# Optimization experiments

Measured on AMD Instinct MI355X. Metric: run time of the kernel, lower is better.

Reference implementation:

```python
import jax, jax.numpy as jnp
import numpy as np

B, NQ, NK, D, H, DH = 4, 2048, 2048, 512, 8, 64  # inner_dim = H*DH = 512 = query_dim


def setup_inputs() -> dict:
    key = jax.random.key(0)
    ks = jax.random.split(key, 9)
    s = 0.02
    return {
        "init_query": jax.random.normal(ks[0], (B, NQ, D), dtype=jnp.float32),
        "embedding": jax.random.normal(ks[1], (B, NK, D), dtype=jnp.float32),
        "Wq": jax.random.normal(ks[2], (D, H * DH), dtype=jnp.float32) * s,
        "Wk": jax.random.normal(ks[3], (D, H * DH), dtype=jnp.float32) * s,
        "Wv": jax.random.normal(ks[4], (D, H * DH), dtype=jnp.float32) * s,
        "W0": jax.random.normal(ks[5], (H * DH, D), dtype=jnp.float32) * s,
        "b0": jnp.zeros((D,), dtype=jnp.float32),
        "W1": jax.random.normal(ks[6], (D, D), dtype=jnp.float32) * s,
        "b1": jnp.zeros((D,), dtype=jnp.float32),
    }


def reference(init_query, embedding, Wq, Wk, Wv, W0, b0, W1, b1):
    b, nq, _ = init_query.shape
    nk = embedding.shape[1]
    # project and split heads -> [b, h, n, dh]
    q = (init_query @ Wq).reshape(b, nq, H, DH).transpose(0, 2, 1, 3)
    k = (embedding @ Wk).reshape(b, nk, H, DH).transpose(0, 2, 1, 3)
    v = (embedding @ Wv).reshape(b, nk, H, DH).transpose(0, 2, 1, 3)
    # offset attention: alpha=1 (no 1/sqrt(d) scale)
    scores = jnp.einsum("bhqd,bhkd->bhqk", q, k)
    # softmax over the QUERY axis (torch dim=1 of [B*H, Nq, Nk]), then renormalize rows
    probs = jax.nn.softmax(scores, axis=2)
    probs = probs / (1e-12 + probs.sum(axis=-1, keepdims=True))
    out = jnp.einsum("bhqk,bhkd->bhqd", probs, v)
    out = out.transpose(0, 2, 1, 3).reshape(b, nq, H * DH)  # merge heads
    out = init_query - (out @ W0 + b0)  # offset residual
    out = out @ W1 + b1  # final projection (dropout p=0 -> identity)
    return out
```

## Files before the change

kernel.cpp:

```cpp
#include <hip/hip_runtime.h>
#include <math.h>

#define BATCH 4
#define NQ 2048
#define NKEY 2048
#define DMODEL 512
#define NH 8
#define DHEAD 64
#define BH (BATCH * NH)

typedef __attribute__((ext_vector_type(8))) short short8;
typedef __attribute__((ext_vector_type(4))) float f32x4;

#define MFMA16(a, b, c) __builtin_amdgcn_mfma_f32_16x16x32_bf16((a), (b), (c), 0, 0, 0)

static __device__ __forceinline__ unsigned short f2b(float f) {
    union { float f; unsigned u; } v; v.f = f;
    unsigned r = (v.u + 0x7fffu + ((v.u >> 16) & 1u)) >> 16;
    return (unsigned short)r;
}
static __device__ __forceinline__ float b2f(unsigned short u) {
    union { unsigned u; float f; } v; v.u = ((unsigned)u) << 16;
    return v.f;
}

__launch_bounds__(256) __global__
void cast_x(const float* __restrict__ a, const float* __restrict__ b,
            unsigned short* __restrict__ da, unsigned short* __restrict__ db) {
    const float* s = blockIdx.y ? b : a;
    unsigned short* d = blockIdx.y ? db : da;
    size_t i = ((size_t)blockIdx.x * 256 + threadIdx.x) * 4;
    float4 v = *(const float4*)(s + i);
    ushort4 o;
    o.x = f2b(v.x); o.y = f2b(v.y); o.z = f2b(v.z); o.w = f2b(v.w);
    *(ushort4*)(d + i) = o;
}

__launch_bounds__(256) __global__
void trans_w(const float* __restrict__ w0, const float* __restrict__ w1,
             const float* __restrict__ w2, const float* __restrict__ w3,
             const float* __restrict__ w4, unsigned short* __restrict__ dst) {
    const float* src = (blockIdx.z == 0) ? w0 : (blockIdx.z == 1) ? w1 :
                       (blockIdx.z == 2) ? w2 : (blockIdx.z == 3) ? w3 : w4;
    unsigned short* out = dst + (size_t)blockIdx.z * DMODEL * DMODEL;
    __shared__ float t[32][33];
    const int tx = threadIdx.x & 31, ty = threadIdx.x >> 5;
    const int k0 = blockIdx.x * 32, n0 = blockIdx.y * 32;
    #pragma unroll
    for (int j = 0; j < 4; ++j)
        t[ty + j * 8][tx] = src[(size_t)(k0 + ty + j * 8) * DMODEL + n0 + tx];
    __syncthreads();
    #pragma unroll
    for (int j = 0; j < 4; ++j)
        out[(size_t)(n0 + ty + j * 8) * DMODEL + k0 + tx] = f2b(t[tx][ty + j * 8]);
}

__device__ __forceinline__
void gemm_core(const unsigned short* __restrict__ A0,
               const unsigned short* __restrict__ B0,
               int K, int tid, unsigned short* Al, unsigned short* Bl,
               f32x4 acc[2][4]) {
    const int w = tid >> 6, lane = tid & 63;
    const int l16 = lane & 15, q4 = lane >> 4;
    char* AlB = (char*)Al;
    char* BlB = (char*)Bl;
    const int srow = tid >> 3;
    const int scolb = (tid & 7) * 16;
    const int skoff = (tid & 7) * 8;

    f32x4 z = {0.f, 0.f, 0.f, 0.f};
    #pragma unroll
    for (int i = 0; i < 2; ++i)
        #pragma unroll
        for (int t = 0; t < 4; ++t) acc[i][t] = z;

    short8 ast[4], bst[2];
    #pragma unroll
    for (int c = 0; c < 4; ++c)
        ast[c] = *(const short8*)(A0 + (size_t)(c * 32 + srow) * K + skoff);
    #pragma unroll
    for (int c = 0; c < 2; ++c)
        bst[c] = *(const short8*)(B0 + (size_t)(c * 32 + srow) * K + skoff);

    for (int k0 = 0; k0 < K; k0 += 64) {
        __syncthreads();
        #pragma unroll
        for (int c = 0; c < 4; ++c) {
            const int row = c * 32 + srow;
            *(short8*)(AlB + row * 128 + (scolb ^ ((row & 7) << 4))) = ast[c];
        }
        #pragma unroll
        for (int c = 0; c < 2; ++c) {
            const int row = c * 32 + srow;
            *(short8*)(BlB + row * 128 + (scolb ^ ((row & 7) << 4))) = bst[c];
        }
        if (k0 + 64 < K) {
            #pragma unroll
            for (int c = 0; c < 4; ++c)
                ast[c] = *(const short8*)(A0 + (size_t)(c * 32 + srow) * K + k0 + 64 + skoff);
            #pragma unroll
            for (int c = 0; c < 2; ++c)
                bst[c] = *(const short8*)(B0 + (size_t)(c * 32 + srow) * K + k0 + 64 + skoff);
        }
        __syncthreads();

        #pragma unroll
        for (int kk = 0; kk < 2; ++kk) {
            const int kb = kk * 64;
            const int rswA0 = ((w * 32 + l16) & 7) << 4;
            short8 a0 = *(const short8*)(AlB + (w * 32 + l16) * 128 + ((kb + q4 * 16) ^ rswA0));
            short8 a1 = *(const short8*)(AlB + (w * 32 + 16 + l16) * 128 + ((kb + q4 * 16) ^ rswA0));
            short8 bfr[4];
            #pragma unroll
            for (int t = 0; t < 4; ++t) {
                const int row = t * 16 + l16;
                bfr[t] = *(const short8*)(BlB + row * 128 + ((kb + q4 * 16) ^ ((row & 7) << 4)));
            }
            #pragma unroll
            for (int t = 0; t < 4; ++t) {
                acc[0][t] = MFMA16(a0, bfr[t], acc[0][t]);
                acc[1][t] = MFMA16(a1, bfr[t], acc[1][t]);
            }
        }
    }
}

__launch_bounds__(256) __global__
void gemm_qkv(const unsigned short* __restrict__ Xq,
              const unsigned short* __restrict__ Xe,
              const unsigned short* __restrict__ Wt,
              unsigned short* __restrict__ Qh,
              unsigned short* __restrict__ Kh,
              unsigned short* __restrict__ Vtb) {
    __shared__ unsigned short Al[128 * 64];
    __shared__ unsigned short Bl[64 * 64];
    const int tid = threadIdx.x;
    const int zsel = blockIdx.z;
    const int K = DMODEL;
    const unsigned short* A = (zsel == 0) ? Xq : Xe;
    const unsigned short* B0 = Wt + (size_t)zsel * DMODEL * DMODEL + (size_t)(blockIdx.y * 64) * K;
    const unsigned short* A0 = A + (size_t)(blockIdx.x * 128) * K;

    f32x4 acc[2][4];
    gemm_core(A0, B0, K, tid, Al, Bl, acc);

    const int w = tid >> 6, lane = tid & 63;
    const int l16 = lane & 15, q4 = lane >> 4;
    const int mBase = blockIdx.x * 128 + w * 32;
    const int n0 = blockIdx.y * 64;

    if (zsel < 2) {
        unsigned short* out = (zsel == 0) ? Qh : Kh;
        #pragma unroll
        for (int i = 0; i < 2; ++i)
            #pragma unroll
            for (int t = 0; t < 4; ++t)
                #pragma unroll
                for (int r = 0; r < 4; ++r) {
                    const int m = mBase + i * 16 + q4 * 4 + r;
                    const int n = n0 + t * 16 + l16;
                    out[(((size_t)(m >> 11) * NH + (n >> 6)) * NQ + (m & 2047)) * DHEAD + (n & 63)] = f2b(acc[i][t][r]);
                }
    } else {
        #pragma unroll
        for (int i = 0; i < 2; ++i)
            #pragma unroll
            for (int t = 0; t < 4; ++t) {
                const int m0 = mBase + i * 16 + q4 * 4;
                const int n = n0 + t * 16 + l16;
                ushort4 p;
                p.x = f2b(acc[i][t][0]); p.y = f2b(acc[i][t][1]);
                p.z = f2b(acc[i][t][2]); p.w = f2b(acc[i][t][3]);
                *(ushort4*)(Vtb + (((size_t)(m0 >> 11) * NH + (n >> 6)) * DHEAD + (n & 63)) * NKEY + (m0 & 2047)) = p;
            }
    }
}

template <int MODE>
__launch_bounds__(256) __global__
void gemm_bf16(const unsigned short* __restrict__ A,
               const unsigned short* __restrict__ Bt,
               void* __restrict__ Cout, const float* __restrict__ bias,
               const float* __restrict__ resid, int M, int N, int K) {
    __shared__ unsigned short Al[128 * 64];
    __shared__ unsigned short Bl[64 * 64];
    const int tid = threadIdx.x;
    const unsigned short* A0 = A + (size_t)(blockIdx.x * 128) * K;
    const unsigned short* B0 = Bt + (size_t)(blockIdx.y * 64) * K;

    f32x4 acc[2][4];
    gemm_core(A0, B0, K, tid, Al, Bl, acc);

    const int w = tid >> 6, lane = tid & 63;
    const int l16 = lane & 15, q4 = lane >> 4;
    const int mBase = blockIdx.x * 128 + w * 32;
    const int n0 = blockIdx.y * 64;

    #pragma unroll
    for (int i = 0; i < 2; ++i)
        #pragma unroll
        for (int t = 0; t < 4; ++t)
            #pragma unroll
            for (int r = 0; r < 4; ++r) {
                const int m = mBase + i * 16 + q4 * 4 + r;
                const int n = n0 + t * 16 + l16;
                float v = acc[i][t][r];
                if (MODE == 2) {
                    ((unsigned short*)Cout)[(size_t)m * N + n] = f2b(resid[(size_t)m * N + n] - (v + bias[n]));
                } else {
                    ((float*)Cout)[(size_t)m * N + n] = v + bias[n];
                }
            }
}

__launch_bounds__(512) __global__
void attn_pass1(const unsigned short* __restrict__ Qh,
                const unsigned short* __restrict__ Kh,
                float* __restrict__ colSrcp,
                unsigned short* __restrict__ cbuf) {
    __shared__ unsigned short Qt[2][64 * 64];
    const int tid = threadIdx.x;
    const int w = tid >> 6, lane = tid & 63;
    const int l16 = lane & 15, q4 = lane >> 4;
    const int bh = blockIdx.y;
    const int kcol0 = blockIdx.x * 128 + w * 16;

    short8 bk0, bk1;
    {
        const unsigned short* Krow = Kh + ((size_t)bh * NKEY + kcol0 + l16) * DHEAD;
        bk0 = *(const short8*)(Krow + q4 * 8);
        bk1 = *(const short8*)(Krow + 32 + q4 * 8);
    }
    const unsigned short* Qb = Qh + (size_t)bh * NQ * DHEAD;
    const int srow = tid >> 3;
    const int skoff = (tid & 7) * 8;
    const int ssw = ((tid & 7) * 16) ^ ((srow & 7) << 4);
    const int rsw = (l16 & 7) << 4;

    f32x4 z = {0.f, 0.f, 0.f, 0.f};
    float csum = 0.f;

    short8 qst = *(const short8*)(Qb + (size_t)srow * DHEAD + skoff);
    *(short8*)((char*)Qt[0] + srow * 128 + ssw) = qst;
    qst = *(const short8*)(Qb + (size_t)(64 + srow) * DHEAD + skoff);
    __syncthreads();

    for (int it = 0; it < 32; ++it) {
        const int q0 = it * 64;
        char* QtB = (char*)Qt[it & 1];
        char* QtN = (char*)Qt[(it & 1) ^ 1];

        if (it < 31) {
            *(short8*)(QtN + srow * 128 + ssw) = qst;
            if (it < 30)
                qst = *(const short8*)(Qb + (size_t)(q0 + 128 + srow) * DHEAD + skoff);
        }

        #pragma unroll
        for (int qi = 0; qi < 4; ++qi) {
            const int row = qi * 16 + l16;
            short8 a0 = *(const short8*)(QtB + row * 128 + ((q4 * 16) ^ rsw));
            short8 a1 = *(const short8*)(QtB + row * 128 + ((64 + q4 * 16) ^ rsw));
            __builtin_amdgcn_s_setprio(1);
            f32x4 s = MFMA16(a0, bk0, z);
            s = MFMA16(a1, bk1, s);
            __builtin_amdgcn_s_setprio(0);
            csum += __expf(s[0]) + __expf(s[1]) + __expf(s[2]) + __expf(s[3]);
        }
        __syncthreads();
    }
    csum += __shfl_xor(csum, 16, 64);
    csum += __shfl_xor(csum, 32, 64);
    if (q4 == 0) {
        const float c = 1.0f / csum;
        colSrcp[(size_t)bh * NKEY + kcol0 + l16] = c;
        cbuf[(size_t)bh * NKEY + kcol0 + l16] = f2b(c);
    }
}

__launch_bounds__(256) __global__
void scale_v(unsigned short* __restrict__ Vtb, const float* __restrict__ colSrcp) {
    const size_t t8 = ((size_t)blockIdx.x * 256 + threadIdx.x) * 8;
    const int k = (int)(t8 & (NKEY - 1));
    const int bh = (int)(t8 >> 17);
    const float* cs = colSrcp + ((size_t)bh << 11) + k;
    short8 v = *(const short8*)(Vtb + t8);
    float4 c0 = *(const float4*)cs;
    float4 c1 = *(const float4*)(cs + 4);
    short8 o;
    o[0] = (short)f2b(b2f((unsigned short)v[0]) * c0.x);
    o[1] = (short)f2b(b2f((unsigned short)v[1]) * c0.y);
    o[2] = (short)f2b(b2f((unsigned short)v[2]) * c0.z);
    o[3] = (short)f2b(b2f((unsigned short)v[3]) * c0.w);
    o[4] = (short)f2b(b2f((unsigned short)v[4]) * c1.x);
    o[5] = (short)f2b(b2f((unsigned short)v[5]) * c1.y);
    o[6] = (short)f2b(b2f((unsigned short)v[6]) * c1.z);
    o[7] = (short)f2b(b2f((unsigned short)v[7]) * c1.w);
    *(short8*)(Vtb + t8) = o;
}

__launch_bounds__(512) __global__
void attn_pass2(const unsigned short* __restrict__ Qh,
                const unsigned short* __restrict__ Kh,
                const unsigned short* __restrict__ Vt,
                const unsigned short* __restrict__ cb,
                unsigned short* __restrict__ attnb) {
    __shared__ unsigned short Kt[2][64 * 64];
    __shared__ unsigned short Vtile[2][64 * 64];
    __shared__ unsigned short Elds[8][16][40];
    const int tid = threadIdx.x;
    const int w = tid >> 6, lane = tid & 63;
    const int l16 = lane & 15, q4 = lane >> 4;
    const int bh = blockIdx.y;
    const int b = bh >> 3, h = bh & 7;
    const int q0w = blockIdx.x * 128 + w * 16;

    short8 aq0, aq1;
    {
        const unsigned short* Qrow = Qh + ((size_t)bh * NQ + q0w + l16) * DHEAD;
        aq0 = *(const short8*)(Qrow + q4 * 8);
        aq1 = *(const short8*)(Qrow + 32 + q4 * 8);
    }
    const unsigned short* Kb = Kh + (size_t)bh * NKEY * DHEAD;
    const unsigned short* Vb = Vt + (size_t)bh * DHEAD * NKEY;
    const unsigned short* cbb = cb + (size_t)bh * NKEY;
    char* Ew = (char*)&Elds[w][0][0];

    const int srow = tid >> 3;
    const int skoff = (tid & 7) * 8;
    const int ssw = ((tid & 7) * 16) ^ ((srow & 7) << 4);
    const int rsw = (l16 & 7) << 4;

    f32x4 z = {0.f, 0.f, 0.f, 0.f};
    f32x4 o[4];
    #pragma unroll
    for (int t = 0; t < 4; ++t) o[t] = z;
    f32x4 o5 = z;

    short8 kst = *(const short8*)(Kb + (size_t)srow * DHEAD + skoff);
    short8 vst = *(const short8*)(Vb + (size_t)srow * NKEY + skoff);
    *(short8*)((char*)Kt[0] + srow * 128 + ssw) = kst;
    *(short8*)((char*)Vtile[0] + srow * 128 + ssw) = vst;
    kst = *(const short8*)(Kb + (size_t)(64 + srow) * DHEAD + skoff);
    vst = *(const short8*)(Vb + (size_t)srow * NKEY + 64 + skoff);
    __syncthreads();

    for (int it = 0; it < 32; ++it) {
        const int k0 = it * 64;
        char* KtB = (char*)Kt[it & 1];
        char* VtB = (char*)Vtile[it & 1];
        char* KtN = (char*)Kt[(it & 1) ^ 1];
        char* VtN = (char*)Vtile[(it & 1) ^ 1];

        if (it < 31) {
            *(short8*)(KtN + srow * 128 + ssw) = kst;
            *(short8*)(VtN + srow * 128 + ssw) = vst;
            if (it < 30) {
                kst = *(const short8*)(Kb + (size_t)(k0 + 128 + srow) * DHEAD + skoff);
                vst = *(const short8*)(Vb + (size_t)srow * NKEY + (k0 + 128) + skoff);
            }
        }

        #pragma unroll
        for (int sub = 0; sub < 2; ++sub) {
            const int kb = k0 + sub * 32;
            short8 bk[2][2];
            #pragma unroll
            for (int jt = 0; jt < 2; ++jt) {
                const int row = sub * 32 + jt * 16 + l16;
                bk[jt][0] = *(const short8*)(KtB + row * 128 + ((q4 * 16) ^ rsw));
                bk[jt][1] = *(const short8*)(KtB + row * 128 + ((64 + q4 * 16) ^ rsw));
            }
            short8 bv[4];
            #pragma unroll
            for (int t = 0; t < 4; ++t) {
                const int row = t * 16 + l16;
                bv[t] = *(const short8*)(VtB + row * 128 + ((sub * 64 + q4 * 16) ^ rsw));
            }
            short8 bv5 = *(const short8*)(cbb + kb + q4 * 8);

            #pragma unroll
            for (int jt = 0; jt < 2; ++jt) {
                __builtin_amdgcn_s_setprio(1);
                f32x4 st = MFMA16(bk[jt][0], aq0, z);
                st = MFMA16(bk[jt][1], aq1, st);
                __builtin_amdgcn_s_setprio(0);
                uint2 p;
                p.x = (unsigned)f2b(__expf(st[0])) | ((unsigned)f2b(__expf(st[1])) << 16);
                p.y = (unsigned)f2b(__expf(st[2])) | ((unsigned)f2b(__expf(st[3])) << 16);
                *(uint2*)(Ew + l16 * 80 + jt * 32 + q4 * 8) = p;
            }
            short8 ea = *(const short8*)(Ew + l16 * 80 + q4 * 16);
            __builtin_amdgcn_s_setprio(1);
            #pragma unroll
            for (int t = 0; t < 4; ++t)
                o[t] = MFMA16(ea, bv[t], o[t]);
            o5 = MFMA16(ea, bv5, o5);
            __builtin_amdgcn_s_setprio(0);
        }
        __syncthreads();
    }

    float rr[4];
    #pragma unroll
    for (int r = 0; r < 4; ++r) rr[r] = 1.0f / (1e-12f + o5[r]);
    #pragma unroll
    for (int t = 0; t < 4; ++t)
        #pragma unroll
        for (int r = 0; r < 4; ++r) {
            const int q = q0w + q4 * 4 + r;
            attnb[((size_t)b * NQ + q) * DMODEL + h * DHEAD + t * 16 + l16] =
                f2b(o[t][r] * rr[r]);
        }
}

extern "C" void kernel_launch(void* const* d_in, const int* in_sizes, int n_in,
                              void* d_out, int out_size, void* d_ws, size_t ws_size,
                              hipStream_t stream) {
    const float* init_query = (const float*)d_in[0];
    const float* embedding  = (const float*)d_in[1];
    const float* Wq = (const float*)d_in[2];
    const float* Wk = (const float*)d_in[3];
    const float* Wv = (const float*)d_in[4];
    const float* W0 = (const float*)d_in[5];
    const float* b0 = (const float*)d_in[6];
    const float* W1 = (const float*)d_in[7];
    const float* b1 = (const float*)d_in[8];
    float* out = (float*)d_out;

    const size_t ACT = (size_t)BATCH * NQ * DMODEL;
    const size_t WEL = (size_t)DMODEL * DMODEL;

    unsigned short* Xq   = (unsigned short*)d_ws;
    unsigned short* Xe   = Xq + ACT;
    unsigned short* Wt   = Xe + ACT;
    unsigned short* Qh   = Wt + 5 * WEL;
    unsigned short* Kh   = Qh + ACT;
    unsigned short* Vtb  = Kh + ACT;
    unsigned short* attnb= Vtb + ACT;
    unsigned short* ybuf = attnb + ACT;
    float* colSrcp = (float*)(ybuf + ACT);

    unsigned short* cbuf = ybuf;

    unsigned short* W0t = Wt + 3 * WEL;
    unsigned short* W1t = Wt + 4 * WEL;

    const int M = BATCH * NQ;
    dim3 blk(256);
    dim3 blk512(512);
    dim3 gGemm(M / 128, DMODEL / 64);

    cast_x<<<dim3(ACT / 1024, 2), blk, 0, stream>>>(init_query, embedding, Xq, Xe);
    trans_w<<<dim3(16, 16, 5), blk, 0, stream>>>(Wq, Wk, Wv, W0, W1, Wt);

    gemm_qkv<<<dim3(M / 128, DMODEL / 64, 3), blk, 0, stream>>>(Xq, Xe, Wt, Qh, Kh, Vtb);

    attn_pass1<<<dim3(NKEY / 128, BH), blk512, 0, stream>>>(Qh, Kh, colSrcp, cbuf);
    scale_v<<<dim3(ACT / 2048), blk, 0, stream>>>(Vtb, colSrcp);
    attn_pass2<<<dim3(NQ / 128, BH), blk512, 0, stream>>>(Qh, Kh, Vtb, cbuf, attnb);

    gemm_bf16<2><<<gGemm, blk, 0, stream>>>(attnb, W0t, ybuf, b0, init_query, M, DMODEL, DMODEL);
    gemm_bf16<3><<<gGemm, blk, 0, stream>>>(ybuf, W1t, out, b1, nullptr, M, DMODEL, DMODEL);
}
```

Measured before the change: 226.1 us.

## Double-buffer GEMM LDS, fold log2e into Wq, use exp2 and packed bf16 cvt

```diff
diff --git a/kernel.cpp b/kernel.cpp
--- a/kernel.cpp
+++ b/kernel.cpp
@@ -22,6 +22,14 @@
 static __device__ __forceinline__ float b2f(unsigned short u) {
     union { unsigned u; float f; } v; v.u = ((unsigned)u) << 16;
     return v.f;
+}
+static __device__ __forceinline__ unsigned pkbf(float lo, float hi) {
+    unsigned r;
+    asm("v_cvt_pk_bf16_f32 %0, %1, %2" : "=v"(r) : "v"(lo), "v"(hi));
+    return r;
+}
+static __device__ __forceinline__ float ex2(float x) {
+    return __builtin_amdgcn_exp2f(x);
 }
 
 __launch_bounds__(256) __global__
@@ -43,6 +51,7 @@
     const float* src = (blockIdx.z == 0) ? w0 : (blockIdx.z == 1) ? w1 :
                        (blockIdx.z == 2) ? w2 : (blockIdx.z == 3) ? w3 : w4;
     unsigned short* out = dst + (size_t)blockIdx.z * DMODEL * DMODEL;
+    const float sc = (blockIdx.z == 0) ? 1.44269504088896340736f : 1.0f;
     __shared__ float t[32][33];
     const int tx = threadIdx.x & 31, ty = threadIdx.x >> 5;
     const int k0 = blockIdx.x * 32, n0 = blockIdx.y * 32;
@@ -52,7 +61,7 @@
     __syncthreads();
     #pragma unroll
     for (int j = 0; j < 4; ++j)
-        out[(size_t)(n0 + ty + j * 8) * DMODEL + k0 + tx] = f2b(t[tx][ty + j * 8]);
+        out[(size_t)(n0 + ty + j * 8) * DMODEL + k0 + tx] = f2b(t[tx][ty + j * 8] * sc);
 }
 
 __device__ __forceinline__
@@ -62,8 +71,6 @@
                f32x4 acc[2][4]) {
     const int w = tid >> 6, lane = tid & 63;
     const int l16 = lane & 15, q4 = lane >> 4;
-    char* AlB = (char*)Al;
-    char* BlB = (char*)Bl;
     const int srow = tid >> 3;
     const int scolb = (tid & 7) * 16;
     const int skoff = (tid & 7) * 8;
@@ -81,9 +88,9 @@
     #pragma unroll
     for (int c = 0; c < 2; ++c)
         bst[c] = *(const short8*)(B0 + (size_t)(c * 32 + srow) * K + skoff);
-
-    for (int k0 = 0; k0 < K; k0 += 64) {
-        __syncthreads();
+    {
+        char* AlB = (char*)Al;
+        char* BlB = (char*)Bl;
         #pragma unroll
         for (int c = 0; c < 4; ++c) {
             const int row = c * 32 + srow;
@@ -94,15 +101,42 @@
             const int row = c * 32 + srow;
             *(short8*)(BlB + row * 128 + (scolb ^ ((row & 7) << 4))) = bst[c];
         }
-        if (k0 + 64 < K) {
-            #pragma unroll
-            for (int c = 0; c < 4; ++c)
-                ast[c] = *(const short8*)(A0 + (size_t)(c * 32 + srow) * K + k0 + 64 + skoff);
-            #pragma unroll
-            for (int c = 0; c < 2; ++c)
-                bst[c] = *(const short8*)(B0 + (size_t)(c * 32 + srow) * K + k0 + 64 + skoff);
-        }
-        __syncthreads();
+    }
+    #pragma unroll
+    for (int c = 0; c < 4; ++c)
+        ast[c] = *(const short8*)(A0 + (size_t)(c * 32 + srow) * K + 64 + skoff);
+    #pragma unroll
+    for (int c = 0; c < 2; ++c)
+        bst[c] = *(const short8*)(B0 + (size_t)(c * 32 + srow) * K + 64 + skoff);
+    __syncthreads();
+
+    const int NT = K >> 6;
+    for (int t = 0; t < NT; ++t) {
+        char* AlB = (char*)(Al + (t & 1) * (128 * 64));
+        char* BlB = (char*)(Bl + (t & 1) * (64 * 64));
+        if (t + 1 < NT) {
+            char* AlN = (char*)(Al + ((t + 1) & 1) * (128 * 64));
+            char* BlN = (char*)(Bl + ((t + 1) & 1) * (64 * 64));
+            #pragma unroll
+            for (int c = 0; c < 4; ++c) {
+                const int row = c * 32 + srow;
+                *(short8*)(AlN + row * 128 + (scolb ^ ((row & 7) << 4))) = ast[c];
+            }
+            #pragma unroll
+            for (int c = 0; c < 2; ++c) {
+                const int row = c * 32 + srow;
+                *(short8*)(BlN + row * 128 + (scolb ^ ((row & 7) << 4))) = bst[c];
+            }
+            if (t + 2 < NT) {
+                const int kn = (t + 2) * 64;
+                #pragma unroll
+                for (int c = 0; c < 4; ++c)
+                    ast[c] = *(const short8*)(A0 + (size_t)(c * 32 + srow) * K + kn + skoff);
+                #pragma unroll
+                for (int c = 0; c < 2; ++c)
+                    bst[c] = *(const short8*)(B0 + (size_t)(c * 32 + srow) * K + kn + skoff);
+            }
+        }
 
         #pragma unroll
         for (int kk = 0; kk < 2; ++kk) {
@@ -112,16 +146,17 @@
             short8 a1 = *(const short8*)(AlB + (w * 32 + 16 + l16) * 128 + ((kb + q4 * 16) ^ rswA0));
             short8 bfr[4];
             #pragma unroll
-            for (int t = 0; t < 4; ++t) {
-                const int row = t * 16 + l16;
-                bfr[t] = *(const short8*)(BlB + row * 128 + ((kb + q4 * 16) ^ ((row & 7) << 4)));
-            }
-            #pragma unroll
-            for (int t = 0; t < 4; ++t) {
-                acc[0][t] = MFMA16(a0, bfr[t], acc[0][t]);
-                acc[1][t] = MFMA16(a1, bfr[t], acc[1][t]);
-            }
-        }
+            for (int t2 = 0; t2 < 4; ++t2) {
+                const int row = t2 * 16 + l16;
+                bfr[t2] = *(const short8*)(BlB + row * 128 + ((kb + q4 * 16) ^ ((row & 7) << 4)));
+            }
+            #pragma unroll
+            for (int t2 = 0; t2 < 4; ++t2) {
+                acc[0][t2] = MFMA16(a0, bfr[t2], acc[0][t2]);
+                acc[1][t2] = MFMA16(a1, bfr[t2], acc[1][t2]);
+            }
+        }
+        __syncthreads();
     }
 }
 
@@ -132,8 +167,8 @@
               unsigned short* __restrict__ Qh,
               unsigned short* __restrict__ Kh,
               unsigned short* __restrict__ Vtb) {
-    __shared__ unsigned short Al[128 * 64];
-    __shared__ unsigned short Bl[64 * 64];
+    __shared__ unsigned short Al[2][128 * 64];
+    __shared__ unsigned short Bl[2][64 * 64];
     const int tid = threadIdx.x;
     const int zsel = blockIdx.z;
     const int K = DMODEL;
@@ -142,7 +177,7 @@
     const unsigned short* A0 = A + (size_t)(blockIdx.x * 128) * K;
 
     f32x4 acc[2][4];
-    gemm_core(A0, B0, K, tid, Al, Bl, acc);
+    gemm_core(A0, B0, K, tid, &Al[0][0], &Bl[0][0], acc);
 
     const int w = tid >> 6, lane = tid & 63;
     const int l16 = lane & 15, q4 = lane >> 4;
@@ -182,14 +217,14 @@
                const unsigned short* __restrict__ Bt,
                void* __restrict__ Cout, const float* __restrict__ bias,
                const float* __restrict__ resid, int M, int N, int K) {
-    __shared__ unsigned short Al[128 * 64];
-    __shared__ unsigned short Bl[64 * 64];
+    __shared__ unsigned short Al[2][128 * 64];
+    __shared__ unsigned short Bl[2][64 * 64];
     const int tid = threadIdx.x;
     const unsigned short* A0 = A + (size_t)(blockIdx.x * 128) * K;
     const unsigned short* B0 = Bt + (size_t)(blockIdx.y * 64) * K;
 
     f32x4 acc[2][4];
-    gemm_core(A0, B0, K, tid, Al, Bl, acc);
+    gemm_core(A0, B0, K, tid, &Al[0][0], &Bl[0][0], acc);
 
     const int w = tid >> 6, lane = tid & 63;
     const int l16 = lane & 15, q4 = lane >> 4;
@@ -218,7 +253,7 @@
                 const unsigned short* __restrict__ Kh,
                 float* __restrict__ colSrcp,
                 unsigned short* __restrict__ cbuf) {
-    __shared__ unsigned short Qt[2][64 * 64];
+    __shared__ unsigned short Qt[2][128 * 64];
     const int tid = threadIdx.x;
     const int w = tid >> 6, lane = tid & 63;
     const int l16 = lane & 15, q4 = lane >> 4;
@@ -240,24 +275,30 @@
     f32x4 z = {0.f, 0.f, 0.f, 0.f};
     float csum = 0.f;
 
-    short8 qst = *(const short8*)(Qb + (size_t)srow * DHEAD + skoff);
-    *(short8*)((char*)Qt[0] + srow * 128 + ssw) = qst;
-    qst = *(const short8*)(Qb + (size_t)(64 + srow) * DHEAD + skoff);
+    short8 qa = *(const short8*)(Qb + (size_t)srow * DHEAD + skoff);
+    short8 qb = *(const short8*)(Qb + (size_t)(64 + srow) * DHEAD + skoff);
+    *(short8*)((char*)Qt[0] + srow * 128 + ssw) = qa;
+    *(short8*)((char*)Qt[0] + (64 + srow) * 128 + ssw) = qb;
+    qa = *(const short8*)(Qb + (size_t)(128 + srow) * DHEAD + skoff);
+    qb = *(const short8*)(Qb + (size_t)(192 + srow) * DHEAD + skoff);
     __syncthreads();
 
-    for (int it = 0; it < 32; ++it) {
-        const int q0 = it * 64;
+    for (int it = 0; it < 16; ++it) {
+        const int q0 = it * 128;
         char* QtB = (char*)Qt[it & 1];
         char* QtN = (char*)Qt[(it & 1) ^ 1];
 
-        if (it < 31) {
-            *(short8*)(QtN + srow * 128 + ssw) = qst;
-            if (it < 30)
-                qst = *(const short8*)(Qb + (size_t)(q0 + 128 + srow) * DHEAD + skoff);
-        }
-
-        #pragma unroll
-        for (int qi = 0; qi < 4; ++qi) {
+        if (it < 15) {
+            *(short8*)(QtN + srow * 128 + ssw) = qa;
+            *(short8*)(QtN + (64 + srow) * 128 + ssw) = qb;
+            if (it < 14) {
+                qa = *(const short8*)(Qb + (size_t)(q0 + 256 + srow) * DHEAD + skoff);
+                qb = *(const short8*)(Qb + (size_t)(q0 + 320 + srow) * DHEAD + skoff);
+            }
+        }
+
+        #pragma unroll
+        for (int qi = 0; qi < 8; ++qi) {
             const int row = qi * 16 + l16;
             short8 a0 = *(const short8*)(QtB + row * 128 + ((q4 * 16) ^ rsw));
             short8 a1 = *(const short8*)(QtB + row * 128 + ((64 + q4 * 16) ^ rsw));
@@ -265,7 +306,7 @@
             f32x4 s = MFMA16(a0, bk0, z);
             s = MFMA16(a1, bk1, s);
             __builtin_amdgcn_s_setprio(0);
-            csum += __expf(s[0]) + __expf(s[1]) + __expf(s[2]) + __expf(s[3]);
+            csum += ex2(s[0]) + ex2(s[1]) + ex2(s[2]) + ex2(s[3]);
         }
         __syncthreads();
     }
@@ -305,8 +346,8 @@
                 const unsigned short* __restrict__ Vt,
                 const unsigned short* __restrict__ cb,
                 unsigned short* __restrict__ attnb) {
-    __shared__ unsigned short Kt[2][64 * 64];
-    __shared__ unsigned short Vtile[2][64 * 64];
+    __shared__ unsigned short Kt[2][128 * 64];
+    __shared__ unsigned short Vg[2][2][64 * 64];
     __shared__ unsigned short Elds[8][16][40];
     const int tid = threadIdx.x;
     const int w = tid >> 6, lane = tid & 63;
@@ -337,33 +378,48 @@
     for (int t = 0; t < 4; ++t) o[t] = z;
     f32x4 o5 = z;
 
-    short8 kst = *(const short8*)(Kb + (size_t)srow * DHEAD + skoff);
-    short8 vst = *(const short8*)(Vb + (size_t)srow * NKEY + skoff);
-    *(short8*)((char*)Kt[0] + srow * 128 + ssw) = kst;
-    *(short8*)((char*)Vtile[0] + srow * 128 + ssw) = vst;
-    kst = *(const short8*)(Kb + (size_t)(64 + srow) * DHEAD + skoff);
-    vst = *(const short8*)(Vb + (size_t)srow * NKEY + 64 + skoff);
+    short8 kst[2], vst[2];
+    kst[0] = *(const short8*)(Kb + (size_t)srow * DHEAD + skoff);
+    kst[1] = *(const short8*)(Kb + (size_t)(64 + srow) * DHEAD + skoff);
+    vst[0] = *(const short8*)(Vb + (size_t)srow * NKEY + skoff);
+    vst[1] = *(const short8*)(Vb + (size_t)srow * NKEY + 64 + skoff);
+    {
+        char* K0 = (char*)&Kt[0][0];
+        char* V0 = (char*)&Vg[0][0][0];
+        *(short8*)(K0 + srow * 128 + ssw) = kst[0];
+        *(short8*)(K0 + (64 + srow) * 128 + ssw) = kst[1];
+        *(short8*)(V0 + srow * 128 + ssw) = vst[0];
+        *(short8*)(V0 + 8192 + srow * 128 + ssw) = vst[1];
+    }
+    kst[0] = *(const short8*)(Kb + (size_t)(128 + srow) * DHEAD + skoff);
+    kst[1] = *(const short8*)(Kb + (size_t)(192 + srow) * DHEAD + skoff);
+    vst[0] = *(const short8*)(Vb + (size_t)srow * NKEY + 128 + skoff);
+    vst[1] = *(const short8*)(Vb + (size_t)srow * NKEY + 192 + skoff);
     __syncthreads();
 
-    for (int it = 0; it < 32; ++it) {
-        const int k0 = it * 64;
-        char* KtB = (char*)Kt[it & 1];
-        char* VtB = (char*)Vtile[it & 1];
-        char* KtN = (char*)Kt[(it & 1) ^ 1];
-        char* VtN = (char*)Vtile[(it & 1) ^ 1];
-
-        if (it < 31) {
-            *(short8*)(KtN + srow * 128 + ssw) = kst;
-            *(short8*)(VtN + srow * 128 + ssw) = vst;
-            if (it < 30) {
-                kst = *(const short8*)(Kb + (size_t)(k0 + 128 + srow) * DHEAD + skoff);
-                vst = *(const short8*)(Vb + (size_t)srow * NKEY + (k0 + 128) + skoff);
-            }
-        }
-
-        #pragma unroll
-        for (int sub = 0; sub < 2; ++sub) {
-            const int kb = k0 + sub * 32;
+    for (int it = 0; it < 16; ++it) {
+        const int kb = it * 128;
+        char* KtB = (char*)&Kt[it & 1][0];
+        char* VgB = (char*)&Vg[it & 1][0][0];
+
+        if (it < 15) {
+            char* KtN = (char*)&Kt[(it & 1) ^ 1][0];
+            char* VgN = (char*)&Vg[(it & 1) ^ 1][0][0];
+            *(short8*)(KtN + srow * 128 + ssw) = kst[0];
+            *(short8*)(KtN + (64 + srow) * 128 + ssw) = kst[1];
+            *(short8*)(VgN + srow * 128 + ssw) = vst[0];
+            *(short8*)(VgN + 8192 + srow * 128 + ssw) = vst[1];
+            if (it < 14) {
+                const int kn = kb + 256;
+                kst[0] = *(const short8*)(Kb + (size_t)(kn + srow) * DHEAD + skoff);
+                kst[1] = *(const short8*)(Kb + (size_t)(kn + 64 + srow) * DHEAD + skoff);
+                vst[0] = *(const short8*)(Vb + (size_t)srow * NKEY + kn + skoff);
+                vst[1] = *(const short8*)(Vb + (size_t)srow * NKEY + kn + 64 + skoff);
+            }
+        }
+
+        #pragma unroll
+        for (int sub = 0; sub < 4; ++sub) {
             short8 bk[2][2];
             #pragma unroll
             for (int jt = 0; jt < 2; ++jt) {
@@ -375,9 +431,10 @@
             #pragma unroll
             for (int t = 0; t < 4; ++t) {
                 const int row = t * 16 + l16;
-                bv[t] = *(const short8*)(VtB + row * 128 + ((sub * 64 + q4 * 16) ^ rsw));
-            }
-            short8 bv5 = *(const short8*)(cbb + kb + q4 * 8);
+                bv[t] = *(const short8*)(VgB + (sub >> 1) * 8192 + row * 128 +
+                                         (((sub & 1) * 64 + q4 * 16) ^ rsw));
+            }
+            short8 bv5 = *(const short8*)(cbb + kb + sub * 32 + q4 * 8);
 
             #pragma unroll
             for (int jt = 0; jt < 2; ++jt) {
@@ -386,8 +443,8 @@
                 st = MFMA16(bk[jt][1], aq1, st);
                 __builtin_amdgcn_s_setprio(0);
                 uint2 p;
-                p.x = (unsigned)f2b(__expf(st[0])) | ((unsigned)f2b(__expf(st[1])) << 16);
-                p.y = (unsigned)f2b(__expf(st[2])) | ((unsigned)f2b(__expf(st[3])) << 16);
+                p.x = pkbf(ex2(st[0]), ex2(st[1]));
+                p.y = pkbf(ex2(st[2]), ex2(st[3]));
                 *(uint2*)(Ew + l16 * 80 + jt * 32 + q4 * 8) = p;
             }
             short8 ea = *(const short8*)(Ew + l16 * 80 + q4 * 16);
```

Measured after the change: 209.3 us. 7.4% less time.
